# Optimization experiments

Hardware: AMD Instinct MI355X
Metric: run time of the kernel (lower is better)

## Reference

```python
import jax, jax.numpy as jnp
import numpy as np

N = 1024  # codeword length (power of 2)
K = 512   # info bits
BATCH = 65536
NB_STAGES = int(np.log2(N))  # 10


def _gen_indices(n):
    """Stage-wise gather indices; index n points at a sentinel zero column."""
    nb_stages = int(np.log2(n))
    ind_gather = np.full((nb_stages, n + 1), n, dtype=np.int32)
    for s in range(nb_stages):
        ind_range = np.arange(n // 2)
        ind_dest = ind_range * 2 - np.mod(ind_range, 2 ** s)
        ind_gather[s, ind_dest] = ind_dest + 2 ** s
    return ind_gather


def setup_inputs() -> dict:
    key = jax.random.key(0)
    # binary information bits, float32 as in the original layer
    u = jax.random.randint(key, (BATCH, K), 0, 2).astype(jnp.float32)
    frozen_pos = np.arange(N - K)
    info_pos = jnp.asarray(np.setdiff1d(np.arange(N), frozen_pos), dtype=jnp.int32)  # [K]
    ind_gather = jnp.asarray(_gen_indices(N))  # [NB_STAGES, N+1]
    return {"u": u, "info_pos": info_pos, "ind_gather": ind_gather}


def reference(u, info_pos, ind_gather) -> jnp.ndarray:
    b = u.shape[0]
    # scatter info bits into codeword positions; frozen positions stay 0
    c = jnp.zeros((b, N), u.dtype).at[:, info_pos].set(u)
    # append sentinel zero column at index N (gather target for pass-through lanes)
    x = jnp.concatenate([c, jnp.zeros((b, 1), u.dtype)], axis=1)  # [b, N+1]
    # log2(N)-stage butterfly: XOR == add mod 2 for binary values
    for s in range(NB_STAGES):
        x = jnp.mod(x + x[:, ind_gather[s]], 2.0)
    return x[:, :N]
```

## Files before the change

### kernel.cpp

```cpp
#include <hip/hip_runtime.h>


#define PN     1024
#define PK     512
#define PBATCH 65536
#define WORDS  32

__global__ __launch_bounds__(256) void polar_encode_kernel(
    const float* __restrict__ u,
    const int*   __restrict__ info_pos,
    float*       __restrict__ out)
{
    __shared__ int   inv[PN];
    __shared__ float su[4][2 * PK];
    const int tid = threadIdx.x;
    #pragma unroll
    for (int i = tid; i < PN; i += 256) inv[i] = -1;
    __syncthreads();
    #pragma unroll
    for (int k = tid; k < PK; k += 256) inv[info_pos[k]] = k;
    __syncthreads();

    const int lane = tid & 63;
    const int wave = tid >> 6;
    const int l31  = lane & 31;
    const int half = lane >> 5;
    const unsigned rA = blockIdx.x * 8u + wave * 2u;

    {
        const float4* u4  = (const float4*)(u + (size_t)rA * PK);
        float4*       su4 = (float4*)su[wave];
        #pragma unroll
        for (int j = 0; j < 4; ++j)
            su4[j * 64 + lane] = u4[j * 64 + lane];
    }

    const float* srow = su[wave] + half * PK;
    unsigned int word = 0;
    #pragma unroll
    for (int c = 0; c < WORDS; ++c) {
        const int   iv  = inv[c * 32 + l31];
        const float v   = srow[iv & (PK - 1)];
        const bool  bit = (iv >= 0) && (v != 0.0f);
        const unsigned long long m = __ballot(bit);
        const unsigned int sel =
            half ? (unsigned int)(m >> 32) : (unsigned int)m;
        if (l31 == c) word = sel;
    }

    word ^= (word >> 1)  & 0x55555555u;
    word ^= (word >> 2)  & 0x33333333u;
    word ^= (word >> 4)  & 0x0F0F0F0Fu;
    word ^= (word >> 8)  & 0x00FF00FFu;
    word ^= (word >> 16) & 0x0000FFFFu;

    #pragma unroll
    for (int off = 1; off <= 16; off <<= 1) {
        const unsigned int partner =
            (unsigned int)__shfl_xor((int)word, off, 64);
        if ((l31 & off) == 0) word ^= partner;
    }

    float4* out4 = (float4*)out;
    const unsigned base = rA * (PN / 4);
    #pragma unroll
    for (int j = 0; j < 8; ++j) {
        const int f   = j * 64 + lane;
        const int r   = f >> 8;
        const int wir = (f & 255) >> 3;
        const int src = wir + (r << 5);
        const unsigned int b   = (unsigned int)__shfl((int)word, src, 64);
        const unsigned int nib = (b >> ((lane & 7) * 4)) & 0xFu;
        float4 v4;
        v4.x = (nib & 1u) ? 1.0f : 0.0f;
        v4.y = (nib & 2u) ? 1.0f : 0.0f;
        v4.z = (nib & 4u) ? 1.0f : 0.0f;
        v4.w = (nib & 8u) ? 1.0f : 0.0f;
        out4[base + f] = v4;
    }
}

extern "C" void kernel_launch(void* const* d_in, const int* in_sizes, int n_in,
                              void* d_out, int out_size, void* d_ws, size_t ws_size,
                              hipStream_t stream) {
    const float* u        = (const float*)d_in[0];
    const int*   info_pos = (const int*)d_in[1];
    float* out = (float*)d_out;

    const int blocks = PBATCH / 8;
    polar_encode_kernel<<<blocks, 256, 0, stream>>>(u, info_pos, out);
}
```

Measured before the change: 359.4 us.

## Precompute inverse index map in workspace, one row per wave, nontemporal stores

Builds the inverse info-position map once in a small pre-kernel in workspace instead of per block in shared memory, when workspace is large enough. Each wave now encodes one row rather than two, so the grid has twice as many blocks. Output float4 stores become nontemporal. The aim is to drop the per-block shared-memory setup and its two barriers and to avoid polluting the cache with the write-only output. The cost is an extra kernel launch and inverse lookups that now read global memory (L1/L2 cached) instead of LDS.

```diff
diff --git a/kernel.cpp b/kernel.cpp
--- a/kernel.cpp
+++ b/kernel.cpp
@@ -4,48 +4,47 @@
 #define PN     1024
 #define PK     512
 #define PBATCH 65536
-#define WORDS  32
+#define ROUNDS 16
 
-__global__ __launch_bounds__(256) void polar_encode_kernel(
-    const float* __restrict__ u,
-    const int*   __restrict__ info_pos,
-    float*       __restrict__ out)
+typedef float vf4 __attribute__((ext_vector_type(4)));
+
+__global__ __launch_bounds__(256) void build_inv_kernel(
+    const int* __restrict__ info_pos, int* __restrict__ inv)
 {
-    __shared__ int   inv[PN];
-    __shared__ float su[4][2 * PK];
     const int tid = threadIdx.x;
     #pragma unroll
     for (int i = tid; i < PN; i += 256) inv[i] = -1;
     __syncthreads();
     #pragma unroll
     for (int k = tid; k < PK; k += 256) inv[info_pos[k]] = k;
-    __syncthreads();
+}
 
-    const int lane = tid & 63;
-    const int wave = tid >> 6;
-    const int l31  = lane & 31;
-    const int half = lane >> 5;
-    const unsigned rA = blockIdx.x * 8u + wave * 2u;
+__device__ __forceinline__ void encode_row(
+    const float* __restrict__ u,
+    const int*   __restrict__ inv,
+    float*       __restrict__ srow,
+    vf4*         __restrict__ out4,
+    int lane, unsigned row)
+{
+    const float4* u4 = (const float4*)(u + (size_t)row * PK);
+    const float4 a0 = u4[lane];
+    const float4 a1 = u4[64 + lane];
+    float4* s4 = (float4*)srow;
+    s4[lane]      = a0;
+    s4[64 + lane] = a1;
 
-    {
-        const float4* u4  = (const float4*)(u + (size_t)rA * PK);
-        float4*       su4 = (float4*)su[wave];
-        #pragma unroll
-        for (int j = 0; j < 4; ++j)
-            su4[j * 64 + lane] = u4[j * 64 + lane];
-    }
+    const int l31 = lane & 31;
 
-    const float* srow = su[wave] + half * PK;
     unsigned int word = 0;
     #pragma unroll
-    for (int c = 0; c < WORDS; ++c) {
-        const int   iv  = inv[c * 32 + l31];
+    for (int c = 0; c < ROUNDS; ++c) {
+        const int   iv  = inv[c * 64 + lane];
         const float v   = srow[iv & (PK - 1)];
         const bool  bit = (iv >= 0) && (v != 0.0f);
         const unsigned long long m = __ballot(bit);
         const unsigned int sel =
-            half ? (unsigned int)(m >> 32) : (unsigned int)m;
-        if (l31 == c) word = sel;
+            (l31 & 1) ? (unsigned int)(m >> 32) : (unsigned int)m;
+        if ((l31 >> 1) == c) word = sel;
     }
 
     word ^= (word >> 1)  & 0x55555555u;
@@ -61,23 +60,54 @@
         if ((l31 & off) == 0) word ^= partner;
     }
 
-    float4* out4 = (float4*)out;
-    const unsigned base = rA * (PN / 4);
+    const unsigned base = row * (PN / 4);
     #pragma unroll
-    for (int j = 0; j < 8; ++j) {
+    for (int j = 0; j < 4; ++j) {
         const int f   = j * 64 + lane;
-        const int r   = f >> 8;
-        const int wir = (f & 255) >> 3;
-        const int src = wir + (r << 5);
+        const int src = f >> 3;
         const unsigned int b   = (unsigned int)__shfl((int)word, src, 64);
-        const unsigned int nib = (b >> ((lane & 7) * 4)) & 0xFu;
-        float4 v4;
-        v4.x = (nib & 1u) ? 1.0f : 0.0f;
-        v4.y = (nib & 2u) ? 1.0f : 0.0f;
-        v4.z = (nib & 4u) ? 1.0f : 0.0f;
-        v4.w = (nib & 8u) ? 1.0f : 0.0f;
-        out4[base + f] = v4;
+        const unsigned int nib = (b >> ((f & 7) * 4)) & 0xFu;
+        vf4 v;
+        v.x = (nib & 1u) ? 1.0f : 0.0f;
+        v.y = (nib & 2u) ? 1.0f : 0.0f;
+        v.z = (nib & 4u) ? 1.0f : 0.0f;
+        v.w = (nib & 8u) ? 1.0f : 0.0f;
+        __builtin_nontemporal_store(v, out4 + base + f);
     }
+}
+
+__global__ __launch_bounds__(256) void polar_encode_kernel(
+    const float* __restrict__ u,
+    const int*   __restrict__ ginv,
+    vf4*         __restrict__ out4)
+{
+    __shared__ float su[4][PK];
+    const int tid  = threadIdx.x;
+    const int lane = tid & 63;
+    const int wave = tid >> 6;
+    const unsigned row = blockIdx.x * 4u + wave;
+    encode_row(u, ginv, su[wave], out4, lane, row);
+}
+
+__global__ __launch_bounds__(256) void polar_fused_kernel(
+    const float* __restrict__ u,
+    const int*   __restrict__ info_pos,
+    vf4*         __restrict__ out4)
+{
+    __shared__ int   inv[PN];
+    __shared__ float su[4][PK];
+    const int tid = threadIdx.x;
+    #pragma unroll
+    for (int i = tid; i < PN; i += 256) inv[i] = -1;
+    __syncthreads();
+    #pragma unroll
+    for (int k = tid; k < PK; k += 256) inv[info_pos[k]] = k;
+    __syncthreads();
+
+    const int lane = tid & 63;
+    const int wave = tid >> 6;
+    const unsigned row = blockIdx.x * 4u + wave;
+    encode_row(u, inv, su[wave], out4, lane, row);
 }
 
 extern "C" void kernel_launch(void* const* d_in, const int* in_sizes, int n_in,
@@ -85,8 +115,13 @@
                               hipStream_t stream) {
     const float* u        = (const float*)d_in[0];
     const int*   info_pos = (const int*)d_in[1];
-    float* out = (float*)d_out;
+    vf4* out4 = (vf4*)d_out;
 
-    const int blocks = PBATCH / 8;
-    polar_encode_kernel<<<blocks, 256, 0, stream>>>(u, info_pos, out);
+    if (ws_size >= (size_t)PN * 4) {
+        int* inv = (int*)d_ws;
+        build_inv_kernel<<<1, 256, 0, stream>>>(info_pos, inv);
+        polar_encode_kernel<<<PBATCH / 4, 256, 0, stream>>>(u, inv, out4);
+    } else {
+        polar_fused_kernel<<<PBATCH / 4, 256, 0, stream>>>(u, info_pos, out4);
+    }
 }
```

Result: no change. 355.8 us (-1.0%).
